# Kernel optimization log

Measured on AMD Instinct MI355X. Metric: run time of the kernel, lower is better.

The kernel has to match this reference:

```python
import jax, jax.numpy as jnp
import numpy as np

GAMMA, ALPHA = 2.0, 0.25
MATCH_THR, BKG_THR = 0.5, 0.4  # fastai match_anchors defaults
SCALE = jnp.array([0.1, 0.1, 0.2, 0.2], dtype=jnp.float32)


def cthw2tlbr(b):
    c, s = b[..., :2], b[..., 2:]
    return jnp.concatenate([c - s / 2, c + s / 2], -1)


def tlbr2cthw(b):
    tl, br = b[..., :2], b[..., 2:]
    return jnp.concatenate([(tl + br) / 2, br - tl], -1)


def iou_cthw(anc, tgt):
    # anc [A,4], tgt [T,4], cthw -> [A,T]
    a, t = cthw2tlbr(anc), cthw2tlbr(tgt)
    tl = jnp.maximum(a[:, None, :2], t[None, :, :2])
    br = jnp.minimum(a[:, None, 2:], t[None, :, 2:])
    sz = jnp.clip(br - tl, 0.0)
    inter = sz[..., 0] * sz[..., 1]
    union = (anc[:, 2] * anc[:, 3])[:, None] + (tgt[:, 2] * tgt[:, 3])[None, :] - inter
    return inter / (union + 1e-8)


def one_image(cp, bp, ct, bt, anchors):
    # cp [A,C], bp [A,4], ct [T] int (0 = pad/background id), bt [T,4] tlbr
    n_classes = cp.shape[1]
    bt_cthw = tlbr2cthw(bt)
    ious = iou_cthw(anchors, bt_cthw)                       # [A,T]
    vals, idxs = jnp.max(ious, 1), jnp.argmax(ious, 1)
    matches = jnp.where(vals > MATCH_THR, idxs,
                        jnp.where(vals < BKG_THR, -1, -2))  # -2 = ignore
    bbox_mask = matches >= 0
    m = jnp.sum(bbox_mask)
    mf = m.astype(cp.dtype)
    g = bt_cthw[jnp.clip(matches, 0)]                       # [A,4] gathered tgt cthw
    t_ctr = (g[:, :2] - anchors[:, :2]) / anchors[:, 2:]
    t_sz = jnp.log(g[:, 2:] / anchors[:, 2:] + 1e-8)
    activ = jnp.concatenate([t_ctr, t_sz], -1) / SCALE
    d = bp - activ
    huber = jnp.where(jnp.abs(d) < 1.0, 0.5 * d * d, jnp.abs(d) - 0.5)
    bb_loss = jnp.sum(huber * bbox_mask[:, None]) / jnp.maximum(mf * 4.0, 1.0)
    # classification: background (0) for matches==-1, gathered class for matches>=0
    cls = jnp.where(bbox_mask, ct[jnp.clip(matches, 0)], 0)  # [A]
    clas_mask = (matches >= -1).astype(cp.dtype)             # drop ignored anchors
    tgt = jax.nn.one_hot(cls - 1, n_classes, dtype=cp.dtype) # cls==0 -> all-zero row
    ps = jax.nn.sigmoid(cp)
    w = (tgt * (1 - ps) + (1 - tgt) * ps) ** GAMMA * ((1 - tgt) * ALPHA + tgt * (1 - ALPHA))
    bce = tgt * jax.nn.softplus(-cp) + (1 - tgt) * jax.nn.softplus(cp)
    focal = jnp.sum(w * bce * clas_mask[:, None]) / jnp.maximum(mf, 1.0)
    return bb_loss, focal


def setup_inputs() -> dict:
    key = jax.random.key(0)
    B, A, C, T = 16, 49152, 80, 64
    k1, k2, k3, k4, k5, k6, k7 = jax.random.split(key, 7)
    clas_preds = jax.random.normal(k1, (B, A, C), jnp.float32)
    bbox_preds = jax.random.normal(k2, (B, A, 4), jnp.float32)
    xy1 = jax.random.uniform(k3, (B, T, 2)) * 0.7
    wh = jax.random.uniform(k4, (B, T, 2)) * 0.25 + 0.02
    bbox_tgts = jnp.concatenate([xy1, xy1 + wh], -1)        # tlbr, all valid
    clas_tgts = jax.random.randint(k5, (B, T), 1, C + 1)    # no padding (>=1)
    ctr = jax.random.uniform(k6, (A, 2))
    sz = jax.random.uniform(k7, (A, 2)) * 0.25 + 0.02
    anchors = jnp.concatenate([ctr, sz], -1)                # cthw
    return dict(clas_preds=clas_preds, bbox_preds=bbox_preds,
                bbox_tgts=bbox_tgts, clas_tgts=clas_tgts, anchors=anchors)


def reference(clas_preds, bbox_preds, bbox_tgts, clas_tgts, anchors):
    bb, fl = jax.vmap(lambda cp, bp, ct, bt: one_image(cp, bp, ct, bt, anchors))(
        clas_preds, bbox_preds, clas_tgts, bbox_tgts)
    return (jnp.sum(bb) + jnp.sum(fl)) / clas_preds.shape[0]
```

## Files before the change

### kernel.cpp

```cpp
#include <hip/hip_runtime.h>


#define A_CNT 49152
#define T_CNT 64
#define C_CNT 80
#define ABLK  256
#define NBLK  (A_CNT / ABLK)
#define B_CNT 16
#define NSLOT (B_CNT * NBLK)

#define LN2   0.6931471806f
#define RLN2  1.44269504f

typedef float f32x4 __attribute__((ext_vector_type(4)));

__device__ __forceinline__ float focal_l2(float x) {
    float e  = __builtin_amdgcn_exp2f(x * RLN2);
    float t  = 1.0f + e;
    float ps = e * __builtin_amdgcn_rcpf(t);
    float L  = __builtin_amdgcn_logf(t);
    return ps * ps * L;
}

__global__ __launch_bounds__(ABLK, 4) void rnfl_main(
    const float* __restrict__ clas_preds,
    const float* __restrict__ bbox_preds,
    const float* __restrict__ bbox_tgts,
    const int*   __restrict__ clas_tgts,
    const float* __restrict__ anchors,
    float* __restrict__ bb_part,
    float* __restrict__ fl_part,
    float* __restrict__ flc_part,
    float* __restrict__ m_part)
{
    const int tid  = threadIdx.x;
    const int role = blockIdx.x & 1;
    const int bid2 = blockIdx.x >> 1;
    const int b    = bid2 / NBLK;
    const int bx   = bid2 - b * NBLK;
    const int lane = tid & 63, wave = tid >> 6;

    if (role == 0) {
        const f32x4* cp4 = reinterpret_cast<const f32x4*>(clas_preds)
                         + ((size_t)b * A_CNT + bx * ABLK) * (C_CNT / 4);

        float acc0 = 0.0f, acc1 = 0.0f;
#pragma unroll
        for (int k = 0; k < 20; k += 2) {
            f32x4 v0 = __builtin_nontemporal_load(cp4 + (k       * ABLK + tid));
            f32x4 v1 = __builtin_nontemporal_load(cp4 + ((k + 1) * ABLK + tid));
            acc0 += (focal_l2(v0.x) + focal_l2(v0.y)) + (focal_l2(v0.z) + focal_l2(v0.w));
            acc1 += (focal_l2(v1.x) + focal_l2(v1.y)) + (focal_l2(v1.z) + focal_l2(v1.w));
        }
        float fl = (acc0 + acc1) * (0.25f * LN2);

        __shared__ float rfl[4];
#pragma unroll
        for (int off = 32; off > 0; off >>= 1)
            fl += __shfl_down(fl, off);
        if (lane == 0) rfl[wave] = fl;
        __syncthreads();
        if (tid == 0)
            fl_part[b * NBLK + bx] = rfl[0] + rfl[1] + rfl[2] + rfl[3];
        return;
    }

    const int a0 = bx * ABLK;

    __shared__ float4 tbox[T_CNT];
    __shared__ float  taT[T_CNT];
    __shared__ int    tcl[T_CNT];
    __shared__ int    wcnt[4];
    __shared__ int    excl_idx[ABLK];
    __shared__ float  rv[4][4];

    if (tid < T_CNT) {
        float4 bt = reinterpret_cast<const float4*>(bbox_tgts)[b * T_CNT + tid];
        float cx = (bt.x + bt.z) * 0.5f;
        float cy = (bt.y + bt.w) * 0.5f;
        float sx = bt.z - bt.x;
        float sy = bt.w - bt.y;
        float4 tb;
        tb.x = cx - sx * 0.5f;
        tb.y = cy - sy * 0.5f;
        tb.z = cx + sx * 0.5f;
        tb.w = cy + sy * 0.5f;
        tbox[tid] = tb;
        taT[tid]  = (tb.z - tb.x) * (tb.w - tb.y) + 1e-8f;
        tcl[tid]  = clas_tgts[b * T_CNT + tid];
    }
    __syncthreads();

    const int a = a0 + tid;
    float4 anc = reinterpret_cast<const float4*>(anchors)[a];
    const float ax1 = anc.x - anc.z * 0.5f;
    const float ay1 = anc.y - anc.w * 0.5f;
    const float ax2 = anc.x + anc.z * 0.5f;
    const float ay2 = anc.y + anc.w * 0.5f;
    const float areaA = anc.z * anc.w;

    float bn = -1.0f, bd = 1.0f;
    int   bj = 0;
#pragma unroll 8
    for (int j = 0; j < T_CNT; ++j) {
        float4 tb = tbox[j];
        float ix1 = fmaxf(ax1, tb.x);
        float iy1 = fmaxf(ay1, tb.y);
        float ix2 = fminf(ax2, tb.z);
        float iy2 = fminf(ay2, tb.w);
        float w = fmaxf(ix2 - ix1, 0.0f);
        float h = fmaxf(iy2 - iy1, 0.0f);
        float inter = w * h;
        float den = (areaA + taT[j]) - inter;
        if (inter * bd > bn * den) { bn = inter; bd = den; bj = j; }
    }

    const f32x4* cp4b = reinterpret_cast<const f32x4*>(clas_preds)
                      + ((size_t)b * A_CNT + a0) * (C_CNT / 4);

    float bb   = 0.0f;
    float flc  = 0.0f;
    float craw = 0.0f;
    float mloc = 0.0f;
    bool  excl = false;

    if (bn > 0.5f * bd) {
        mloc = 1.0f;
        int code = tcl[bj] - 1;
        float4 tb = tbox[bj];
        float gx = (tb.x + tb.z) * 0.5f;
        float gy = (tb.y + tb.w) * 0.5f;
        float gw = tb.z - tb.x;
        float gh = tb.w - tb.y;
        float4 bp = reinterpret_cast<const float4*>(bbox_preds)[(size_t)b * A_CNT + a];
        float t0 = ((gx - anc.x) / anc.z) * 10.0f;
        float t1 = ((gy - anc.y) / anc.w) * 10.0f;
        float t2 = __logf(gw / anc.z + 1e-8f) * 5.0f;
        float t3 = __logf(gh / anc.w + 1e-8f) * 5.0f;
        float d, ad;
        d = bp.x - t0; ad = fabsf(d); bb += (ad < 1.0f) ? 0.5f * d * d : ad - 0.5f;
        d = bp.y - t1; ad = fabsf(d); bb += (ad < 1.0f) ? 0.5f * d * d : ad - 0.5f;
        d = bp.z - t2; ad = fabsf(d); bb += (ad < 1.0f) ? 0.5f * d * d : ad - 0.5f;
        d = bp.w - t3; ad = fabsf(d); bb += (ad < 1.0f) ? 0.5f * d * d : ad - 0.5f;

        float x  = clas_preds[((size_t)b * A_CNT + a) * C_CNT + code];
        float e  = __builtin_amdgcn_exp2f(x * RLN2);
        float t  = 1.0f + e;
        float inv = __builtin_amdgcn_rcpf(t);
        float ps = e * inv;
        float q  = 1.0f - ps;
        float L  = __builtin_amdgcn_logf(t);
        float sp = LN2 * L;
        flc = 0.75f * q * q * (sp - x) - 0.25f * ps * ps * sp;
    } else {
        excl = (bn >= 0.4f * bd);
    }

    unsigned long long bm = __ballot(excl);
    if (lane == 0) wcnt[wave] = __popcll(bm);
    __syncthreads();
    int wbase = 0;
#pragma unroll
    for (int w = 0; w < 4; ++w) wbase += (w < wave) ? wcnt[w] : 0;
    const int E = wcnt[0] + wcnt[1] + wcnt[2] + wcnt[3];
    if (excl) {
        int rank = wbase + __popcll(bm & ((1ull << lane) - 1ull));
        excl_idx[rank] = tid;
    }
    __syncthreads();

    for (int base = 0; base < E; base += 12) {
        int idx  = base + tid / 20;
        int part = tid % 20;
        if (tid < 240 && idx < E) {
            int al = excl_idx[idx];
            f32x4 v = cp4b[(size_t)al * 20 + part];
            craw -= (focal_l2(v.x) + focal_l2(v.y)) + (focal_l2(v.z) + focal_l2(v.w));
        }
    }

    flc = fmaf(0.25f * LN2, craw, flc);
#pragma unroll
    for (int off = 32; off > 0; off >>= 1) {
        bb   += __shfl_down(bb, off);
        flc  += __shfl_down(flc, off);
        mloc += __shfl_down(mloc, off);
    }
    if (lane == 0) { rv[wave][0] = bb; rv[wave][1] = flc; rv[wave][2] = mloc; }
    __syncthreads();
    if (tid == 0) {
        int slot = b * NBLK + bx;
        bb_part[slot]  = rv[0][0] + rv[1][0] + rv[2][0] + rv[3][0];
        flc_part[slot] = rv[0][1] + rv[1][1] + rv[2][1] + rv[3][1];
        m_part[slot]   = rv[0][2] + rv[1][2] + rv[2][2] + rv[3][2];
    }
}

__global__ __launch_bounds__(256) void rnfl_final(
    const float* __restrict__ bb_part,
    const float* __restrict__ fl_part,
    const float* __restrict__ flc_part,
    const float* __restrict__ m_part,
    float* __restrict__ out)
{
    __shared__ float bbL[NSLOT], flL[NSLOT], fcL[NSLOT], mL[NSLOT];
    __shared__ float wacc[4];
    const int tid = threadIdx.x, lane = tid & 63, wave = tid >> 6;

#pragma unroll
    for (int k = 0; k < NSLOT / 256; ++k) {
        int s = k * 256 + tid;
        bbL[s] = bb_part[s];
        flL[s] = fl_part[s];
        fcL[s] = flc_part[s];
        mL[s]  = m_part[s];
    }
    __syncthreads();

    float lacc = 0.0f;
    for (int img = wave; img < B_CNT; img += 4) {
        float bb = 0.0f, fl = 0.0f, m = 0.0f;
#pragma unroll
        for (int s = 0; s < 3; ++s) {
            int i = img * NBLK + s * 64 + lane;
            bb += bbL[i];
            fl += flL[i] + fcL[i];
            m  += mL[i];
        }
#pragma unroll
        for (int off = 32; off > 0; off >>= 1) {
            bb += __shfl_down(bb, off);
            fl += __shfl_down(fl, off);
            m  += __shfl_down(m, off);
        }
        if (lane == 0)
            lacc += bb / fmaxf(m * 4.0f, 1.0f) + fl / fmaxf(m, 1.0f);
    }
    if (lane == 0) wacc[wave] = lacc;
    __syncthreads();
    if (tid == 0)
        out[0] = (wacc[0] + wacc[1] + wacc[2] + wacc[3]) / (float)B_CNT;
}

extern "C" void kernel_launch(void* const* d_in, const int* in_sizes, int n_in,
                              void* d_out, int out_size, void* d_ws, size_t ws_size,
                              hipStream_t stream)
{
    const float* clas_preds = (const float*)d_in[0];
    const float* bbox_preds = (const float*)d_in[1];
    const float* bbox_tgts  = (const float*)d_in[2];
    const int*   clas_tgts  = (const int*)d_in[3];
    const float* anchors    = (const float*)d_in[4];
    float* out = (float*)d_out;

    float* bb_part  = (float*)d_ws;
    float* fl_part  = bb_part  + NSLOT;
    float* flc_part = fl_part  + NSLOT;
    float* m_part   = flc_part + NSLOT;

    rnfl_main<<<2 * NSLOT, ABLK, 0, stream>>>(clas_preds, bbox_preds, bbox_tgts,
                                              clas_tgts, anchors,
                                              bb_part, fl_part, flc_part, m_part);
    rnfl_final<<<1, 256, 0, stream>>>(bb_part, fl_part, flc_part, m_part, out);
}
```

Before: 68.88 us.

## Fuse dense and correction focal passes into one masked single-block streaming pass

Merges the two block roles into one block per anchor tile. Each block prefetches its class-prediction slab into registers, runs IoU matching, and then computes the focal sum with a per-element mask that skips ignored anchors. This replaces the old second gather-and-subtract pass over excluded anchors and drops the extra partial buffer. It also batches four sigmoid reciprocals into one rcp through a product trick, which adds multiplies and some risk of overflow or precision loss for large inputs. Holding eight float4 values per thread raises register pressure and removes the occupancy hint.

```diff
diff --git a/kernel.cpp b/kernel.cpp
--- a/kernel.cpp
+++ b/kernel.cpp
@@ -14,15 +14,28 @@
 
 typedef float f32x4 __attribute__((ext_vector_type(4)));
 
-__device__ __forceinline__ float focal_l2(float x) {
-    float e  = __builtin_amdgcn_exp2f(x * RLN2);
-    float t  = 1.0f + e;
-    float ps = e * __builtin_amdgcn_rcpf(t);
-    float L  = __builtin_amdgcn_logf(t);
-    return ps * ps * L;
-}
-
-__global__ __launch_bounds__(ABLK, 4) void rnfl_main(
+__device__ __forceinline__ float focal4q(f32x4 v) {
+    float e0 = __builtin_amdgcn_exp2f(v.x * RLN2);
+    float e1 = __builtin_amdgcn_exp2f(v.y * RLN2);
+    float e2 = __builtin_amdgcn_exp2f(v.z * RLN2);
+    float e3 = __builtin_amdgcn_exp2f(v.w * RLN2);
+    float t0 = 1.0f + e0, t1 = 1.0f + e1, t2 = 1.0f + e2, t3 = 1.0f + e3;
+    float t01 = t0 * t1, t23 = t2 * t3;
+    float r   = __builtin_amdgcn_rcpf(t01 * t23);
+    float r01 = r * t23, r23 = r * t01;
+    float s0 = e0 * (r01 * t1);
+    float s1 = e1 * (r01 * t0);
+    float s2 = e2 * (r23 * t3);
+    float s3 = e3 * (r23 * t2);
+    float L0 = __builtin_amdgcn_logf(t0);
+    float L1 = __builtin_amdgcn_logf(t1);
+    float L2 = __builtin_amdgcn_logf(t2);
+    float L3 = __builtin_amdgcn_logf(t3);
+    return ((s0 * s0) * L0 + (s1 * s1) * L1)
+         + ((s2 * s2) * L2 + (s3 * s3) * L3);
+}
+
+__global__ __launch_bounds__(ABLK) void rnfl_main(
     const float* __restrict__ clas_preds,
     const float* __restrict__ bbox_preds,
     const float* __restrict__ bbox_tgts,
@@ -30,49 +43,28 @@
     const float* __restrict__ anchors,
     float* __restrict__ bb_part,
     float* __restrict__ fl_part,
-    float* __restrict__ flc_part,
     float* __restrict__ m_part)
 {
     const int tid  = threadIdx.x;
-    const int role = blockIdx.x & 1;
-    const int bid2 = blockIdx.x >> 1;
-    const int b    = bid2 / NBLK;
-    const int bx   = bid2 - b * NBLK;
+    const int g    = blockIdx.x;
     const int lane = tid & 63, wave = tid >> 6;
-
-    if (role == 0) {
-        const f32x4* cp4 = reinterpret_cast<const f32x4*>(clas_preds)
-                         + ((size_t)b * A_CNT + bx * ABLK) * (C_CNT / 4);
-
-        float acc0 = 0.0f, acc1 = 0.0f;
-#pragma unroll
-        for (int k = 0; k < 20; k += 2) {
-            f32x4 v0 = __builtin_nontemporal_load(cp4 + (k       * ABLK + tid));
-            f32x4 v1 = __builtin_nontemporal_load(cp4 + ((k + 1) * ABLK + tid));
-            acc0 += (focal_l2(v0.x) + focal_l2(v0.y)) + (focal_l2(v0.z) + focal_l2(v0.w));
-            acc1 += (focal_l2(v1.x) + focal_l2(v1.y)) + (focal_l2(v1.z) + focal_l2(v1.w));
-        }
-        float fl = (acc0 + acc1) * (0.25f * LN2);
-
-        __shared__ float rfl[4];
-#pragma unroll
-        for (int off = 32; off > 0; off >>= 1)
-            fl += __shfl_down(fl, off);
-        if (lane == 0) rfl[wave] = fl;
-        __syncthreads();
-        if (tid == 0)
-            fl_part[b * NBLK + bx] = rfl[0] + rfl[1] + rfl[2] + rfl[3];
-        return;
-    }
-
-    const int a0 = bx * ABLK;
+    const int b    = g / NBLK;
+    const int bx   = g - b * NBLK;
+    const int a0   = bx * ABLK;
 
     __shared__ float4 tbox[T_CNT];
     __shared__ float  taT[T_CNT];
     __shared__ int    tcl[T_CNT];
-    __shared__ int    wcnt[4];
-    __shared__ int    excl_idx[ABLK];
+    __shared__ int    codes[ABLK];
     __shared__ float  rv[4][4];
+
+    const f32x4* cp4 = reinterpret_cast<const f32x4*>(clas_preds)
+                     + ((size_t)b * A_CNT + a0) * (C_CNT / 4);
+
+    f32x4 buf[8];
+#pragma unroll
+    for (int i = 0; i < 8; ++i)
+        buf[i] = cp4[i * ABLK + tid];
 
     if (tid < T_CNT) {
         float4 bt = reinterpret_cast<const float4*>(bbox_tgts)[b * T_CNT + tid];
@@ -86,7 +78,7 @@
         tb.z = cx + sx * 0.5f;
         tb.w = cy + sy * 0.5f;
         tbox[tid] = tb;
-        taT[tid]  = (tb.z - tb.x) * (tb.w - tb.y) + 1e-8f;
+        taT[tid]  = sx * sy + 1e-8f;
         tcl[tid]  = clas_tgts[b * T_CNT + tid];
     }
     __syncthreads();
@@ -115,18 +107,14 @@
         if (inter * bd > bn * den) { bn = inter; bd = den; bj = j; }
     }
 
-    const f32x4* cp4b = reinterpret_cast<const f32x4*>(clas_preds)
-                      + ((size_t)b * A_CNT + a0) * (C_CNT / 4);
-
+    int   code;
     float bb   = 0.0f;
     float flc  = 0.0f;
-    float craw = 0.0f;
     float mloc = 0.0f;
-    bool  excl = false;
 
     if (bn > 0.5f * bd) {
         mloc = 1.0f;
-        int code = tcl[bj] - 1;
+        code = tcl[bj] - 1;
         float4 tb = tbox[bj];
         float gx = (tb.x + tb.z) * 0.5f;
         float gy = (tb.y + tb.w) * 0.5f;
@@ -153,57 +141,56 @@
         float sp = LN2 * L;
         flc = 0.75f * q * q * (sp - x) - 0.25f * ps * ps * sp;
     } else {
-        excl = (bn >= 0.4f * bd);
-    }
-
-    unsigned long long bm = __ballot(excl);
-    if (lane == 0) wcnt[wave] = __popcll(bm);
-    __syncthreads();
-    int wbase = 0;
-#pragma unroll
-    for (int w = 0; w < 4; ++w) wbase += (w < wave) ? wcnt[w] : 0;
-    const int E = wcnt[0] + wcnt[1] + wcnt[2] + wcnt[3];
-    if (excl) {
-        int rank = wbase + __popcll(bm & ((1ull << lane) - 1ull));
-        excl_idx[rank] = tid;
-    }
-    __syncthreads();
-
-    for (int base = 0; base < E; base += 12) {
-        int idx  = base + tid / 20;
-        int part = tid % 20;
-        if (tid < 240 && idx < E) {
-            int al = excl_idx[idx];
-            f32x4 v = cp4b[(size_t)al * 20 + part];
-            craw -= (focal_l2(v.x) + focal_l2(v.y)) + (focal_l2(v.z) + focal_l2(v.w));
-        }
-    }
-
-    flc = fmaf(0.25f * LN2, craw, flc);
+        code = (bn >= 0.4f * bd) ? -2 : -1;
+    }
+    codes[tid] = code;
+    __syncthreads();
+
+    unsigned mbits = 0;
+#pragma unroll
+    for (int k = 0; k < 20; ++k) {
+        int al = (unsigned)(k * ABLK + tid) / 20u;
+        mbits |= (codes[al] >= -1 ? 1u : 0u) << k;
+    }
+
+    float acc = 0.0f;
+#pragma unroll
+    for (int k = 0; k < 12; ++k) {
+        f32x4 cur = buf[k & 7];
+        buf[k & 7] = cp4[(k + 8) * ABLK + tid];
+        float m = (float)((mbits >> k) & 1u);
+        acc = fmaf(m, focal4q(cur), acc);
+    }
+#pragma unroll
+    for (int k = 12; k < 20; ++k) {
+        float m = (float)((mbits >> k) & 1u);
+        acc = fmaf(m, focal4q(buf[k & 7]), acc);
+    }
+    float fl = fmaf(acc, 0.25f * LN2, flc);
+
 #pragma unroll
     for (int off = 32; off > 0; off >>= 1) {
         bb   += __shfl_down(bb, off);
-        flc  += __shfl_down(flc, off);
+        fl   += __shfl_down(fl, off);
         mloc += __shfl_down(mloc, off);
     }
-    if (lane == 0) { rv[wave][0] = bb; rv[wave][1] = flc; rv[wave][2] = mloc; }
+    if (lane == 0) { rv[wave][0] = bb; rv[wave][1] = fl; rv[wave][2] = mloc; }
     __syncthreads();
     if (tid == 0) {
         int slot = b * NBLK + bx;
-        bb_part[slot]  = rv[0][0] + rv[1][0] + rv[2][0] + rv[3][0];
-        flc_part[slot] = rv[0][1] + rv[1][1] + rv[2][1] + rv[3][1];
-        m_part[slot]   = rv[0][2] + rv[1][2] + rv[2][2] + rv[3][2];
+        bb_part[slot] = rv[0][0] + rv[1][0] + rv[2][0] + rv[3][0];
+        fl_part[slot] = rv[0][1] + rv[1][1] + rv[2][1] + rv[3][1];
+        m_part[slot]  = rv[0][2] + rv[1][2] + rv[2][2] + rv[3][2];
     }
 }
 
 __global__ __launch_bounds__(256) void rnfl_final(
     const float* __restrict__ bb_part,
     const float* __restrict__ fl_part,
-    const float* __restrict__ flc_part,
     const float* __restrict__ m_part,
     float* __restrict__ out)
 {
-    __shared__ float bbL[NSLOT], flL[NSLOT], fcL[NSLOT], mL[NSLOT];
+    __shared__ float bbL[NSLOT], flL[NSLOT], mL[NSLOT];
     __shared__ float wacc[4];
     const int tid = threadIdx.x, lane = tid & 63, wave = tid >> 6;
 
@@ -212,7 +199,6 @@
         int s = k * 256 + tid;
         bbL[s] = bb_part[s];
         flL[s] = fl_part[s];
-        fcL[s] = flc_part[s];
         mL[s]  = m_part[s];
     }
     __syncthreads();
@@ -224,7 +210,7 @@
         for (int s = 0; s < 3; ++s) {
             int i = img * NBLK + s * 64 + lane;
             bb += bbL[i];
-            fl += flL[i] + fcL[i];
+            fl += flL[i];
             m  += mL[i];
         }
 #pragma unroll
@@ -253,13 +239,12 @@
     const float* anchors    = (const float*)d_in[4];
     float* out = (float*)d_out;
 
-    float* bb_part  = (float*)d_ws;
-    float* fl_part  = bb_part  + NSLOT;
-    float* flc_part = fl_part  + NSLOT;
-    float* m_part   = flc_part + NSLOT;
-
-    rnfl_main<<<2 * NSLOT, ABLK, 0, stream>>>(clas_preds, bbox_preds, bbox_tgts,
-                                              clas_tgts, anchors,
-                                              bb_part, fl_part, flc_part, m_part);
-    rnfl_final<<<1, 256, 0, stream>>>(bb_part, fl_part, flc_part, m_part, out);
-}
+    float* bb_part = (float*)d_ws;
+    float* fl_part = bb_part + NSLOT;
+    float* m_part  = fl_part + NSLOT;
+
+    rnfl_main<<<NSLOT, ABLK, 0, stream>>>(clas_preds, bbox_preds, bbox_tgts,
+                                          clas_tgts, anchors,
+                                          bb_part, fl_part, m_part);
+    rnfl_final<<<1, 256, 0, stream>>>(bb_part, fl_part, m_part, out);
+}
```

New measurement: 56.94 us, median of 2. -17.3%, faster.
